# Optimization experiments

Hardware: AMD Instinct MI355X
Metric: run time of the kernel (lower is better)

The kernel has to match this reference:

```python
import jax, jax.numpy as jnp
import numpy as np

N, E = 50000, 1600000
F_IN, EDGE_DIM, HID, HEADS, NCLS = 64, 16, 128, 4, 40
C = HID // HEADS  # per-head dim = 32


def setup_inputs() -> dict:
    key = jax.random.key(0)
    ks = jax.random.split(key, 20)
    s = 0.1
    inp = {
        'x': jax.random.normal(ks[0], (N, F_IN), jnp.float32),
        'edge_index': jax.random.randint(ks[1], (2, E), 0, N, jnp.int64),
        'edge_attr': jax.random.normal(ks[2], (E, EDGE_DIM), jnp.float32),
        # layer 1 params
        'W1': jax.random.normal(ks[3], (HID, F_IN), jnp.float32) * s,
        'as1': jax.random.normal(ks[4], (HEADS, C), jnp.float32) * s,
        'ad1': jax.random.normal(ks[5], (HEADS, C), jnp.float32) * s,
        'ae1': jax.random.normal(ks[6], (HEADS, C), jnp.float32) * s,
        'We1': jax.random.normal(ks[7], (HID, EDGE_DIM), jnp.float32) * s,
        'b1': jnp.zeros((HID,), jnp.float32),
        # layer 2 params
        'W2': jax.random.normal(ks[8], (HID, HID), jnp.float32) * s,
        'as2': jax.random.normal(ks[9], (HEADS, C), jnp.float32) * s,
        'ad2': jax.random.normal(ks[10], (HEADS, C), jnp.float32) * s,
        'ae2': jax.random.normal(ks[11], (HEADS, C), jnp.float32) * s,
        'We2': jax.random.normal(ks[12], (HID, EDGE_DIM), jnp.float32) * s,
        'b2': jnp.zeros((HID,), jnp.float32),
        # final classifier
        'Wlin': jax.random.normal(ks[13], (NCLS, HID), jnp.float32) * s,
        'blin': jnp.zeros((NCLS,), jnp.float32),
    }
    return inp


def gat_conv(x, src, dst, eattr, W, a_s, a_d, a_e, We, b):
    """PyG GATConv (concat=True, add_self_loops=True, fill_value='mean'), eval mode."""
    n = x.shape[0]
    H, Cd = a_s.shape
    h = (x @ W.T).reshape(n, H, Cd)  # [N,H,C]
    # self-loop edge_attr = per-destination mean of incoming edge_attr
    cnt = jax.ops.segment_sum(jnp.ones((dst.shape[0],), eattr.dtype), dst, num_segments=n)
    mean_ea = jax.ops.segment_sum(eattr, dst, num_segments=n) / jnp.maximum(cnt, 1.0)[:, None]
    loops = jnp.arange(n, dtype=src.dtype)
    s_idx = jnp.concatenate([src, loops])
    d_idx = jnp.concatenate([dst, loops])
    ea = jnp.concatenate([eattr, mean_ea], axis=0)  # [E+N, edge_dim]
    e = (ea @ We.T).reshape(-1, H, Cd)
    # edge-wise attention logits
    alpha = (h * a_s).sum(-1)[s_idx] + (h * a_d).sum(-1)[d_idx] + (e * a_e).sum(-1)  # [E+N,H]
    alpha = jax.nn.leaky_relu(alpha, 0.2)
    # segment softmax over destination neighborhoods (every node has a self-loop)
    amax = jax.ops.segment_max(alpha, d_idx, num_segments=n)
    ex = jnp.exp(alpha - amax[d_idx])
    den = jax.ops.segment_sum(ex, d_idx, num_segments=n)
    coef = ex / (den[d_idx] + 1e-16)
    out = jax.ops.segment_sum(h[s_idx] * coef[:, :, None], d_idx, num_segments=n)
    return out.reshape(n, H * Cd) + b


def reference(x, edge_index, edge_attr, W1, as1, ad1, ae1, We1, b1,
              W2, as2, ad2, ae2, We2, b2, Wlin, blin):
    src, dst = edge_index[0], edge_index[1]
    h = jax.nn.relu(gat_conv(x, src, dst, edge_attr, W1, as1, ad1, ae1, We1, b1))
    h = jax.nn.relu(gat_conv(h, src, dst, edge_attr, W2, as2, ad2, ae2, We2, b2))
    logits = h @ Wlin.T + blin
    return jax.nn.log_softmax(logits, axis=1)
```

## Files before the change

kernel.cpp:

```cpp
#include <hip/hip_runtime.h>
#include <hip/hip_bf16.h>
#include <math.h>


#define CHUNK 2048

typedef __attribute__((ext_vector_type(8))) short short8;
typedef __attribute__((ext_vector_type(4))) float floatx4;
typedef __attribute__((ext_vector_type(2))) float floatx2;

__device__ __forceinline__ unsigned short f2bf(float f) {
  unsigned u = __float_as_uint(f);
  unsigned r = u + 0x7FFFu + ((u >> 16) & 1u);
  return (unsigned short)(r >> 16);
}
__device__ __forceinline__ float bf2f(unsigned short b) {
  return __uint_as_float(((unsigned)b) << 16);
}

__global__ __launch_bounds__(512) void hist_kernel(const int* __restrict__ dst,
                                                   int* __restrict__ bucketCnt,
                                                   int* __restrict__ chunkHist,
                                                   int E, int NB) {
  __shared__ int hist[512];
  const int tid = threadIdx.x;
  hist[tid] = 0;
  __syncthreads();
  const int e0 = blockIdx.x * CHUNK, e1 = min(e0 + CHUNK, E);
  for (int e = e0 + tid; e < e1; e += 512) atomicAdd(&hist[dst[e] >> 7], 1);
  __syncthreads();
  chunkHist[(size_t)blockIdx.x * 512 + tid] = hist[tid];
  if (tid < NB && hist[tid]) atomicAdd(&bucketCnt[tid], hist[tid]);
}

__global__ __launch_bounds__(512) void scanB_kernel(const int* __restrict__ bucketCnt,
                                                    int* __restrict__ bucketOffs,
                                                    int* __restrict__ bucketPos,
                                                    int* __restrict__ offs,
                                                    int NB, int N, int E) {
  __shared__ int sc[512];
  const int tid = threadIdx.x;
  const int v = (tid < NB) ? bucketCnt[tid] : 0;
  sc[tid] = v;
  __syncthreads();
  for (int off = 1; off < 512; off <<= 1) {
    int t = (tid >= off) ? sc[tid - off] : 0;
    __syncthreads();
    sc[tid] += t;
    __syncthreads();
  }
  const int excl = sc[tid] - v;
  if (tid < NB) { bucketOffs[tid] = excl; bucketPos[tid] = excl; }
  if (tid == 0) { bucketOffs[NB] = E; offs[N] = E; }
}

__global__ __launch_bounds__(512) void partB_kernel(const int* __restrict__ src,
                                                    const int* __restrict__ dst,
                                                    const float* __restrict__ ea,
                                                    const float* __restrict__ ae1,
                                                    const float* __restrict__ We1,
                                                    const float* __restrict__ ae2,
                                                    const float* __restrict__ We2,
                                                    const int* __restrict__ chunkHist,
                                                    int* __restrict__ bucketPos,
                                                    int4* __restrict__ binned16,
                                                    int* __restrict__ binned4,
                                                    unsigned char* __restrict__ dlArr,
                                                    int E, int NB) {
  __shared__ float wa[128];
  __shared__ int lbase[513], gbase[512], lcnt[512];
  __shared__ int waveSum[8];
  __shared__ int4 stg16[CHUNK];
  __shared__ int stg4[CHUNK];
  const int tid = threadIdx.x;
  const int wv = tid >> 6;
  const int lane = tid & 63;
  const int e0 = blockIdx.x * CHUNK;
  const int e1 = min(e0 + CHUNK, E);
  lcnt[tid] = 0;
  if (tid < 128) {
    const float* aev = (tid < 64) ? ae1 : ae2;
    const float* Wev = (tid < 64) ? We1 : We2;
    const int h = (tid >> 4) & 3;
    const int d = tid & 15;
    float s = 0.f;
#pragma unroll
    for (int c = 0; c < 32; ++c) s += aev[h * 32 + c] * Wev[(h * 32 + c) * 16 + d];
    wa[tid] = s;
  }
  const int hv = chunkHist[(size_t)blockIdx.x * 512 + tid];
  int v = hv;
#pragma unroll
  for (int off = 1; off < 64; off <<= 1) {
    int t = __shfl_up(v, off);
    if (lane >= off) v += t;
  }
  if (lane == 63) waveSum[wv] = v;
  __syncthreads();
  int woff = 0;
#pragma unroll
  for (int i = 0; i < 8; ++i) woff += (i < wv) ? waveSum[i] : 0;
  const int incl = v + woff;
  lbase[tid + 1] = incl;
  if (tid == 0) lbase[0] = 0;
  if (tid < NB && hv > 0) gbase[tid] = atomicAdd(&bucketPos[tid], hv);
  __syncthreads();
  for (int e = e0 + tid; e < e1; e += 512) {
    const int d = dst[e];
    const int b = d >> 7;
    const int lr = atomicAdd(&lcnt[b], 1);
    const float4* p = (const float4*)(ea + (size_t)e * 16);
    float4 q0 = p[0], q1 = p[1], q2 = p[2], q3 = p[3];
    float v16[16] = {q0.x, q0.y, q0.z, q0.w, q1.x, q1.y, q1.z, q1.w,
                     q2.x, q2.y, q2.z, q2.w, q3.x, q3.y, q3.z, q3.w};
    unsigned short rr[8];
#pragma unroll
    for (int h = 0; h < 8; ++h) {
      float sm = 0.f;
#pragma unroll
      for (int d2 = 0; d2 < 16; ++d2) sm += v16[d2] * wa[h * 16 + d2];
      rr[h] = f2bf(sm);
    }
    int4 pv;
    pv.x = (int)(((unsigned)(src[e] & 0xFFFF)) | ((unsigned)(d & 127) << 16) |
                 ((unsigned)b << 23));
    pv.y = (int)(((unsigned)rr[1] << 16) | rr[0]);
    pv.z = (int)(((unsigned)rr[3] << 16) | rr[2]);
    pv.w = (int)(((unsigned)rr[5] << 16) | rr[4]);
    const int sp = lbase[b] + lr;
    stg16[sp] = pv;
    stg4[sp] = (int)(((unsigned)rr[7] << 16) | rr[6]);
  }
  __syncthreads();
  const int total = e1 - e0;
  for (int t = tid; t < total; t += 512) {
    const int4 pv = stg16[t];
    const int b = (int)(((unsigned)pv.x) >> 23);
    const int g = gbase[b] + (t - lbase[b]);
    binned16[g] = pv;
    binned4[g] = stg4[t];
    dlArr[g] = (unsigned char)((pv.x >> 16) & 127);
  }
}

__global__ __launch_bounds__(256) void passC_kernel(const int4* __restrict__ binned16,
                                                    const int* __restrict__ binned4,
                                                    const unsigned char* __restrict__ dlArr,
                                                    const int* __restrict__ bucketOffs,
                                                    int* __restrict__ srcS,
                                                    uint2* __restrict__ aeS1,
                                                    uint2* __restrict__ aeS2,
                                                    int* __restrict__ offs, int N) {
  __shared__ int cnt[128], dbase[129], dpos[128];
  const int tid = threadIdx.x;
  const int b = blockIdx.x;
  const int bo = bucketOffs[b], be = bucketOffs[b + 1];
  const int m = be - bo;
  if (tid < 128) { cnt[tid] = 0; dpos[tid] = 0; }
  __syncthreads();
  for (int t = tid; t < m; t += 256) atomicAdd(&cnt[dlArr[bo + t]], 1);
  __syncthreads();
  for (int off = 1; off < 128; off <<= 1) {
    int t = (tid < 128 && tid >= (unsigned)off) ? cnt[tid - off] : 0;
    __syncthreads();
    if (tid < 128) cnt[tid] += t;
    __syncthreads();
  }
  if (tid == 0) dbase[0] = 0;
  if (tid < 128) dbase[tid + 1] = cnt[tid];
  __syncthreads();
  const int dcnt = min(128, N - (b << 7));
  if (tid < dcnt) offs[(b << 7) + tid] = bo + dbase[tid];
  for (int t = tid; t < m; t += 256) {
    const int4 v = binned16[bo + t];
    const int w4 = binned4[bo + t];
    const int dl = (v.x >> 16) & 127;
    const int p = dbase[dl] + atomicAdd(&dpos[dl], 1);
    srcS[bo + p] = v.x & 0xFFFF;
    aeS1[bo + p] = make_uint2((unsigned)v.y, (unsigned)v.z);
    aeS2[bo + p] = make_uint2((unsigned)v.w, (unsigned)w4);
  }
}

__global__ __launch_bounds__(256) void cvtall_kernel(const float* __restrict__ W1,
                                                     unsigned short* __restrict__ Wb1,
                                                     const float* __restrict__ W2,
                                                     unsigned short* __restrict__ Wb2,
                                                     const float* __restrict__ Wlin,
                                                     unsigned short* __restrict__ whi,
                                                     unsigned short* __restrict__ wlo) {
  const int n1 = 128 * 64, n2 = 128 * 128, n3 = 48 * 128;
  int i = blockIdx.x * 256 + threadIdx.x;
  if (i < n1) {
    Wb1[i] = f2bf(W1[i]);
  } else if (i < n1 + n2) {
    Wb2[i - n1] = f2bf(W2[i - n1]);
  } else if (i < n1 + n2 + n3) {
    const int j = i - n1 - n2;
    float v = (j < 40 * 128) ? Wlin[j] : 0.f;
    unsigned short h = f2bf(v);
    whi[j] = h;
    wlo[j] = f2bf(v - bf2f(h));
  }
}

#define GEMM_MFMA_SWAPPED(KTOT, PA, PB)                                            \
  {                                                                                \
    for (int kc = 0; kc < (KTOT); kc += 32) {                                      \
      const int koff = kc + (quad << 3);                                           \
      short8 aw[2], bx[4];                                                         \
      _Pragma("unroll") for (int ct = 0; ct < 2; ++ct)                             \
        aw[ct] = *(const short8*)(&Bs[(w * 32 + ct * 16 + l15) * (PB) + koff]);    \
      _Pragma("unroll") for (int nt_ = 0; nt_ < 4; ++nt_)                          \
        bx[nt_] = *(const short8*)(&As[(nt_ * 16 + l15) * (PA) + koff]);           \
      _Pragma("unroll") for (int ct = 0; ct < 2; ++ct)                             \
        _Pragma("unroll") for (int nt_ = 0; nt_ < 4; ++nt_)                        \
          acc[ct][nt_] =                                                           \
              __builtin_amdgcn_mfma_f32_16x16x32_bf16(aw[ct], bx[nt_],             \
                                                      acc[ct][nt_], 0, 0, 0);      \
    }                                                                              \
  }

#define GEMM_WRITE_H_SWAPPED()                                                     \
  {                                                                                \
    _Pragma("unroll") for (int nt_ = 0; nt_ < 4; ++nt_) {                          \
      const int node = m0 + nt_ * 16 + l15;                                        \
      if (node < n) {                                                              \
        _Pragma("unroll") for (int ct = 0; ct < 2; ++ct) {                         \
          const int ch = w * 32 + ct * 16 + (quad << 2);                           \
          ushort4 o;                                                               \
          o.x = f2bf(acc[ct][nt_][0]); o.y = f2bf(acc[ct][nt_][1]);                \
          o.z = f2bf(acc[ct][nt_][2]); o.w = f2bf(acc[ct][nt_][3]);                \
          *(ushort4*)(H + (size_t)node * 128 + ch) = o;                            \
        }                                                                          \
      }                                                                            \
    }                                                                              \
  }

#define GEMM_SCORE_SWAPPED()                                                       \
  {                                                                                \
    float asv[2][4], adv[2][4];                                                    \
    _Pragma("unroll") for (int ct = 0; ct < 2; ++ct)                               \
      _Pragma("unroll") for (int r = 0; r < 4; ++r) {                              \
        const int c = w * 32 + ct * 16 + (quad << 2) + r;                          \
        asv[ct][r] = a_s[c]; adv[ct][r] = a_d[c];                                  \
      }                                                                            \
    _Pragma("unroll") for (int nt_ = 0; nt_ < 4; ++nt_) {                          \
      float ps = 0.f, pd = 0.f;                                                    \
      _Pragma("unroll") for (int ct = 0; ct < 2; ++ct)                             \
        _Pragma("unroll") for (int r = 0; r < 4; ++r) {                            \
          ps += acc[ct][nt_][r] * asv[ct][r];                                      \
          pd += acc[ct][nt_][r] * adv[ct][r];                                      \
        }                                                                          \
      ps += __shfl_xor(ps, 16); ps += __shfl_xor(ps, 32);                          \
      pd += __shfl_xor(pd, 16); pd += __shfl_xor(pd, 32);                          \
      if (lane < 16) {                                                             \
        const int node = m0 + nt_ * 16 + lane;                                     \
        if (node < n) {                                                            \
          ssc[(size_t)node * 4 + w] = ps;                                          \
          dsc[(size_t)node * 4 + w] = pd;                                          \
        }                                                                          \
      }                                                                            \
    }                                                                              \
  }

__global__ __launch_bounds__(256) void gemm_score_f32_kernel(const float* __restrict__ X,
                                                             const unsigned short* __restrict__ Wb,
                                                             const float* __restrict__ a_s,
                                                             const float* __restrict__ a_d,
                                                             unsigned short* __restrict__ H,
                                                             float* __restrict__ ssc,
                                                             float* __restrict__ dsc,
                                                             int n) {
  __shared__ unsigned short As[64 * 72];
  __shared__ unsigned short Bs[128 * 72];
  const int tid = threadIdx.x;
  const int w = tid >> 6;
  const int lane = tid & 63;
  const int m0 = blockIdx.x * 64;
  const int quad = lane >> 4;
  const int l15 = lane & 15;

#pragma unroll
  for (int it = 0; it < 4; ++it) {
    const int idx = it * 256 + tid;
    const int row = idx >> 4;
    const int c4 = (idx & 15) * 4;
    const int grow = min(m0 + row, n - 1);
    const float4 q = *(const float4*)(X + (size_t)grow * 64 + c4);
    unsigned short* dstp = &As[row * 72 + c4];
    dstp[0] = f2bf(q.x); dstp[1] = f2bf(q.y); dstp[2] = f2bf(q.z); dstp[3] = f2bf(q.w);
  }
#pragma unroll
  for (int it = 0; it < 4; ++it) {
    const int idx = it * 256 + tid;
    const int row = idx >> 3;
    const int c8 = (idx & 7) * 8;
    short8 v = *(const short8*)(Wb + (size_t)row * 64 + c8);
    *(short8*)(&Bs[row * 72 + c8]) = v;
  }
  __syncthreads();

  floatx4 acc[2][4];
#pragma unroll
  for (int ct = 0; ct < 2; ++ct)
#pragma unroll
    for (int nt_ = 0; nt_ < 4; ++nt_) acc[ct][nt_] = (floatx4)(0.f);

  GEMM_MFMA_SWAPPED(64, 72, 72)
  GEMM_WRITE_H_SWAPPED()
  GEMM_SCORE_SWAPPED()
}

__global__ __launch_bounds__(256) void gemm_score_kernel(const unsigned short* __restrict__ X,
                                                         const unsigned short* __restrict__ Wb,
                                                         const float* __restrict__ a_s,
                                                         const float* __restrict__ a_d,
                                                         unsigned short* __restrict__ H,
                                                         float* __restrict__ ssc,
                                                         float* __restrict__ dsc,
                                                         int n) {
  __shared__ unsigned short As[64 * 136];
  __shared__ unsigned short Bs[128 * 136];
  const int tid = threadIdx.x;
  const int w = tid >> 6;
  const int lane = tid & 63;
  const int m0 = blockIdx.x * 64;
  const int quad = lane >> 4;
  const int l15 = lane & 15;

#pragma unroll
  for (int it = 0; it < 4; ++it) {
    const int idx = it * 256 + tid;
    const int row = idx >> 4;
    const int c8 = (idx & 15) * 8;
    const int grow = min(m0 + row, n - 1);
    short8 v = *(const short8*)(X + (size_t)grow * 128 + c8);
    *(short8*)(&As[row * 136 + c8]) = v;
  }
#pragma unroll
  for (int it = 0; it < 8; ++it) {
    const int idx = it * 256 + tid;
    const int row = idx >> 4;
    const int c8 = (idx & 15) * 8;
    short8 v = *(const short8*)(Wb + (size_t)row * 128 + c8);
    *(short8*)(&Bs[row * 136 + c8]) = v;
  }
  __syncthreads();

  floatx4 acc[2][4];
#pragma unroll
  for (int ct = 0; ct < 2; ++ct)
#pragma unroll
    for (int nt_ = 0; nt_ < 4; ++nt_) acc[ct][nt_] = (floatx4)(0.f);

  GEMM_MFMA_SWAPPED(128, 136, 136)
  GEMM_WRITE_H_SWAPPED()
  GEMM_SCORE_SWAPPED()
}

__device__ __forceinline__ float leaky02(float a) { return a > 0.f ? a : 0.2f * a; }
__device__ __forceinline__ float sel4(float4 v, int h) {
  return (h == 0) ? v.x : (h == 1) ? v.y : (h == 2) ? v.z : v.w;
}

__global__ __launch_bounds__(256) void agg_kernel(const unsigned short* __restrict__ hin,
                                                  const float* __restrict__ ssc,
                                                  const float* __restrict__ dsc,
                                                  const unsigned short* __restrict__ aeS,
                                                  const int* __restrict__ offs,
                                                  const int* __restrict__ srcS,
                                                  const float* __restrict__ bias,
                                                  unsigned short* __restrict__ hout, int n) {
  __shared__ int sbuf[4][64];
  __shared__ float pbuf[4][256];
  const int tid = threadIdx.x;
  const int wv = tid >> 6;
  const int lane = tid & 63;
  const int node = blockIdx.x * 4 + wv;
  if (node >= n) return;
  const int l32 = lane & 31;
  const int half = lane >> 5;
  const int ch4 = l32 * 4;
  const int headB = l32 >> 3;
  const float4 dv = *(const float4*)(dsc + (size_t)node * 4);
  float4 l4 = make_float4(0.f, 0.f, 0.f, 0.f);
  float4 sa = make_float4(0.f, 0.f, 0.f, 0.f);
  floatx2 acc01 = (floatx2)(0.f);
  floatx2 acc23 = (floatx2)(0.f);
  const int j0 = offs[node], j1 = offs[node + 1];

  for (int jc = j0; jc < j1; jc += 64) {
    const int len = min(64, j1 - jc);
    float4 p4 = make_float4(0.f, 0.f, 0.f, 0.f);
    int sv = 0;
    if (lane < len) {
      const int j = jc + lane;
      sv = srcS[j];
      const ushort4 aq = *(const ushort4*)(aeS + (size_t)j * 4);
      const float4 ae4 = make_float4(bf2f(aq.x), bf2f(aq.y), bf2f(aq.z), bf2f(aq.w));
      const float4 ss4 = *(const float4*)(ssc + (size_t)sv * 4);
      sa.x += ae4.x; sa.y += ae4.y; sa.z += ae4.z; sa.w += ae4.w;
      p4.x = __expf(leaky02(ss4.x + dv.x + ae4.x));
      p4.y = __expf(leaky02(ss4.y + dv.y + ae4.y));
      p4.z = __expf(leaky02(ss4.z + dv.z + ae4.z));
      p4.w = __expf(leaky02(ss4.w + dv.w + ae4.w));
    }
    sbuf[wv][lane] = sv;
    *(float4*)(&pbuf[wv][lane * 4]) = p4;
    l4.x += p4.x; l4.y += p4.y; l4.z += p4.z; l4.w += p4.w;
    int k = 0;
    for (; k + 8 <= len; k += 8) {
      int s[4];
      float p[4];
      uint2 d[4];
#pragma unroll
      for (int u = 0; u < 4; ++u) {
        const int kk = k + 2 * u + half;
        s[u] = sbuf[wv][kk];
        p[u] = pbuf[wv][kk * 4 + headB];
      }
#pragma unroll
      for (int u = 0; u < 4; ++u)
        d[u] = *(const uint2*)(hin + (size_t)s[u] * 128 + ch4);
#pragma unroll
      for (int u = 0; u < 4; ++u) {
        floatx2 p2; p2.x = p[u]; p2.y = p[u];
        floatx2 h01, h23;
        h01.x = __uint_as_float(d[u].x << 16);
        h01.y = __uint_as_float(d[u].x & 0xFFFF0000u);
        h23.x = __uint_as_float(d[u].y << 16);
        h23.y = __uint_as_float(d[u].y & 0xFFFF0000u);
        acc01 += p2 * h01;
        acc23 += p2 * h23;
      }
    }
    for (; k < len; k += 2) {
      int kk = k + half;
      if (kk < len) {
        int s = sbuf[wv][kk];
        float p = pbuf[wv][kk * 4 + headB];
        uint2 d = *(const uint2*)(hin + (size_t)s * 128 + ch4);
        floatx2 p2; p2.x = p; p2.y = p;
        floatx2 h01, h23;
        h01.x = __uint_as_float(d.x << 16);
        h01.y = __uint_as_float(d.x & 0xFFFF0000u);
        h23.x = __uint_as_float(d.y << 16);
        h23.y = __uint_as_float(d.y & 0xFFFF0000u);
        acc01 += p2 * h01;
        acc23 += p2 * h23;
      }
    }
  }

  float acc[4] = {acc01.x, acc01.y, acc23.x, acc23.y};
#pragma unroll
  for (int off = 32; off; off >>= 1) {
    sa.x += __shfl_xor(sa.x, off);
    sa.y += __shfl_xor(sa.y, off);
    sa.z += __shfl_xor(sa.z, off);
    sa.w += __shfl_xor(sa.w, off);
    l4.x += __shfl_xor(l4.x, off);
    l4.y += __shfl_xor(l4.y, off);
    l4.z += __shfl_xor(l4.z, off);
    l4.w += __shfl_xor(l4.w, off);
  }
#pragma unroll
  for (int i = 0; i < 4; ++i) acc[i] += __shfl_xor(acc[i], 32);

  const int deg = j1 - j0;
  const float invd = 1.f / fmaxf((float)deg, 1.f);
  const float ssn = ssc[(size_t)node * 4 + headB];
  const float aloop = leaky02(ssn + sel4(dv, headB) + sel4(sa, headB) * invd);
  const float pl = __expf(aloop);
  const float lF = sel4(l4, headB) + pl;
  const uint2 hd = *(const uint2*)(hin + (size_t)node * 128 + ch4);
  const float hv0 = __uint_as_float(hd.x << 16);
  const float hv1 = __uint_as_float(hd.x & 0xFFFF0000u);
  const float hv2 = __uint_as_float(hd.y << 16);
  const float hv3 = __uint_as_float(hd.y & 0xFFFF0000u);
  const float inv = 1.f / (lF + 1e-16f);
  const float4 bi = *(const float4*)(bias + ch4);
  const float o0 = fmaxf((acc[0] + pl * hv0) * inv + bi.x, 0.f);
  const float o1 = fmaxf((acc[1] + pl * hv1) * inv + bi.y, 0.f);
  const float o2 = fmaxf((acc[2] + pl * hv2) * inv + bi.z, 0.f);
  const float o3 = fmaxf((acc[3] + pl * hv3) * inv + bi.w, 0.f);
  if (half == 0) {
    ushort4 o;
    o.x = f2bf(o0); o.y = f2bf(o1); o.z = f2bf(o2); o.w = f2bf(o3);
    *(ushort4*)(hout + (size_t)node * 128 + ch4) = o;
  }
}

__global__ __launch_bounds__(256) void classifier_kernel(const unsigned short* __restrict__ h,
                                                         const unsigned short* __restrict__ Whi,
                                                         const unsigned short* __restrict__ Wlo,
                                                         const float* __restrict__ blin,
                                                         float* __restrict__ out, int n) {
  const int w = threadIdx.x >> 6;
  const int lane = threadIdx.x & 63;
  const int quad = lane >> 4;
  const int l15 = lane & 15;
  const int row0 = blockIdx.x * 64 + w * 16;
  if (row0 >= n) return;
  int rowm = row0 + l15;
  if (rowm >= n) rowm = n - 1;
  floatx4 acc[3];
#pragma unroll
  for (int nt = 0; nt < 3; ++nt) acc[nt] = (floatx4)(0.f);
  const size_t hbase = (size_t)rowm * 128;
#pragma unroll
  for (int kc = 0; kc < 128; kc += 32) {
    const int koff = kc + (quad << 3);
    short8 a = *(const short8*)(h + hbase + koff);
#pragma unroll
    for (int nt = 0; nt < 3; ++nt) {
      short8 bh = *(const short8*)(Whi + (size_t)(nt * 16 + l15) * 128 + koff);
      short8 bl = *(const short8*)(Wlo + (size_t)(nt * 16 + l15) * 128 + koff);
      acc[nt] = __builtin_amdgcn_mfma_f32_16x16x32_bf16(a, bh, acc[nt], 0, 0, 0);
      acc[nt] = __builtin_amdgcn_mfma_f32_16x16x32_bf16(a, bl, acc[nt], 0, 0, 0);
    }
  }
  const float bl0 = blin[l15];
  const float bl1 = blin[16 + l15];
  const float bl2 = (l15 < 8) ? blin[32 + l15] : 0.f;
#pragma unroll
  for (int r = 0; r < 4; ++r) {
    const int rrow = row0 + (quad << 2) + r;
    const float v0 = acc[0][r] + bl0;
    const float v1 = acc[1][r] + bl1;
    const float v2 = (l15 < 8) ? (acc[2][r] + bl2) : -INFINITY;
    float m = fmaxf(v0, fmaxf(v1, v2));
#pragma unroll
    for (int off = 8; off; off >>= 1) m = fmaxf(m, __shfl_xor(m, off, 16));
    const float e2 = (l15 < 8) ? __expf(v2 - m) : 0.f;
    float s = __expf(v0 - m) + __expf(v1 - m) + e2;
#pragma unroll
    for (int off = 8; off; off >>= 1) s += __shfl_xor(s, off, 16);
    const float ls = m + __logf(s);
    if (rrow < n) {
      float* po = out + (size_t)rrow * 40;
      po[l15] = v0 - ls;
      po[16 + l15] = v1 - ls;
      if (l15 < 8) po[32 + l15] = v2 - ls;
    }
  }
}

extern "C" void kernel_launch(void* const* d_in, const int* in_sizes, int n_in,
                              void* d_out, int out_size, void* d_ws, size_t ws_size,
                              hipStream_t stream) {
  const float* x    = (const float*)d_in[0];
  const int*   eidx = (const int*)d_in[1];
  const float* ea   = (const float*)d_in[2];
  const float* W1   = (const float*)d_in[3];
  const float* as1  = (const float*)d_in[4];
  const float* ad1  = (const float*)d_in[5];
  const float* ae1w = (const float*)d_in[6];
  const float* We1  = (const float*)d_in[7];
  const float* b1   = (const float*)d_in[8];
  const float* W2   = (const float*)d_in[9];
  const float* as2  = (const float*)d_in[10];
  const float* ad2  = (const float*)d_in[11];
  const float* ae2w = (const float*)d_in[12];
  const float* We2  = (const float*)d_in[13];
  const float* b2   = (const float*)d_in[14];
  const float* Wlin = (const float*)d_in[15];
  const float* blin = (const float*)d_in[16];
  float* out = (float*)d_out;

  const int N = in_sizes[0] / 64;
  const int E = in_sizes[1] / 2;
  const int* src = eidx;
  const int* dst = eidx + E;
  const int NB = (N + 127) >> 7;
  const int gp = (E + CHUNK - 1) / CHUNK;

  char* wsb = (char*)d_ws;
  size_t off = 0;
  auto alloc = [&](size_t bytes) -> void* {
    void* p = wsb + off;
    off = (off + bytes + 255) & ~(size_t)255;
    return p;
  };
  int* bucketCnt  = (int*)alloc(512 * 4);
  int* bucketOffs = (int*)alloc(513 * 4);
  int* bucketPos  = (int*)alloc(512 * 4);
  int* offs       = (int*)alloc((size_t)(N + 1) * 4);
  int* chunkHist  = (int*)alloc((size_t)gp * 512 * 4);
  uint2* aeS1     = (uint2*)alloc((size_t)E * 8);
  uint2* aeS2     = (uint2*)alloc((size_t)E * 8);
  void* regC      = alloc((size_t)E * 16);
  int4* binned16  = (int4*)regC;
  unsigned short* hA = (unsigned short*)regC;
  int* binned4    = (int*)alloc((size_t)E * 4);
  unsigned char* dlArr = (unsigned char*)alloc((size_t)E);
  int* srcS       = (int*)alloc((size_t)E * 4);
  unsigned short* Wb1 = (unsigned short*)alloc(128 * 64 * 2);
  unsigned short* Wb2 = (unsigned short*)alloc(128 * 128 * 2);
  unsigned short* Wlh = (unsigned short*)alloc(48 * 128 * 2);
  unsigned short* Wll = (unsigned short*)alloc(48 * 128 * 2);
  float* ssc      = (float*)alloc((size_t)N * 4 * 4);
  float* dsc      = (float*)alloc((size_t)N * 4 * 4);
  unsigned short* hB = (unsigned short*)alloc((size_t)N * 128 * 2);

  const int gg = (N + 63) / 64;
  const int gs = (N + 3) / 4;
  const int ncvt = 128 * 64 + 128 * 128 + 48 * 128;

  hipMemsetAsync(bucketCnt, 0, 512 * 4, stream);
  hist_kernel<<<gp, 512, 0, stream>>>(dst, bucketCnt, chunkHist, E, NB);
  scanB_kernel<<<1, 512, 0, stream>>>(bucketCnt, bucketOffs, bucketPos, offs, NB, N, E);
  partB_kernel<<<gp, 512, 0, stream>>>(src, dst, ea, ae1w, We1, ae2w, We2, chunkHist,
                                       bucketPos, binned16, binned4, dlArr, E, NB);
  passC_kernel<<<NB, 256, 0, stream>>>(binned16, binned4, dlArr, bucketOffs, srcS,
                                       aeS1, aeS2, offs, N);

  cvtall_kernel<<<(ncvt + 255) / 256, 256, 0, stream>>>(W1, Wb1, W2, Wb2, Wlin, Wlh, Wll);

  gemm_score_f32_kernel<<<gg, 256, 0, stream>>>(x, Wb1, as1, ad1, hA, ssc, dsc, N);
  agg_kernel<<<gs, 256, 0, stream>>>(hA, ssc, dsc, (const unsigned short*)aeS1, offs, srcS, b1, hB, N);

  gemm_score_kernel<<<gg, 256, 0, stream>>>(hB, Wb2, as2, ad2, hA, ssc, dsc, N);
  agg_kernel<<<gs, 256, 0, stream>>>(hA, ssc, dsc, (const unsigned short*)aeS2, offs, srcS, b2, hB, N);

  classifier_kernel<<<gg, 256, 0, stream>>>(hB, Wlh, Wll, blin, out, N);
}
```

Baseline: 458.1 us.

## Compute CSR offsets via global degree count and scan; prefetch edges in partB

Replaces the per-bucket local histogram and scan in passC (which read a separate per-edge dlArr byte array) with a global per-node degree count done with atomics, followed by a three-kernel multi-block scan that produces CSR offsets directly. passC then uses these global offsets and drops its shared-memory histogram. partB also software-pipelines its edge loop by loading the next edge's dst, src and attributes before processing the current one. The change removes the dlArr write and read, but adds a 1.6M-atomic count pass, a memset and several small kernel launches.

```diff
diff --git a/kernel.cpp b/kernel.cpp
--- a/kernel.cpp
+++ b/kernel.cpp
@@ -52,6 +52,53 @@
   const int excl = sc[tid] - v;
   if (tid < NB) { bucketOffs[tid] = excl; bucketPos[tid] = excl; }
   if (tid == 0) { bucketOffs[NB] = E; offs[N] = E; }
+}
+
+__global__ __launch_bounds__(256) void countN_kernel(const int* __restrict__ dst,
+                                                     int* __restrict__ cnt, int E) {
+  int i = blockIdx.x * 256 + threadIdx.x;
+  const int stride = gridDim.x * 256;
+  for (; i < E; i += stride) atomicAdd(&cnt[dst[i]], 1);
+}
+
+__global__ __launch_bounds__(256) void scanA_kernel(const int* __restrict__ cnt,
+                                                    int* __restrict__ offs,
+                                                    int* __restrict__ blockSum, int N) {
+  __shared__ int sc[256];
+  const int tid = threadIdx.x;
+  const int i = blockIdx.x * 256 + tid;
+  const int v = (i < N) ? cnt[i] : 0;
+  sc[tid] = v;
+  __syncthreads();
+  for (int off = 1; off < 256; off <<= 1) {
+    int t = (tid >= off) ? sc[tid - off] : 0;
+    __syncthreads();
+    sc[tid] += t;
+    __syncthreads();
+  }
+  if (i < N) offs[i] = sc[tid] - v;
+  if (tid == 255) blockSum[blockIdx.x] = sc[255];
+}
+
+__global__ __launch_bounds__(256) void scanBlk_kernel(int* __restrict__ blockSum, int NBLK) {
+  __shared__ int sc[256];
+  const int tid = threadIdx.x;
+  const int v = (tid < NBLK) ? blockSum[tid] : 0;
+  sc[tid] = v;
+  __syncthreads();
+  for (int off = 1; off < 256; off <<= 1) {
+    int t = (tid >= off) ? sc[tid - off] : 0;
+    __syncthreads();
+    sc[tid] += t;
+    __syncthreads();
+  }
+  if (tid < NBLK) blockSum[tid] = sc[tid] - v;
+}
+
+__global__ __launch_bounds__(256) void finz_kernel(int* __restrict__ offs,
+                                                   const int* __restrict__ blockSum, int N) {
+  const int i = blockIdx.x * 256 + threadIdx.x;
+  if (i < N) offs[i] += blockSum[i >> 8];
 }
 
 __global__ __launch_bounds__(512) void partB_kernel(const int* __restrict__ src,
@@ -65,7 +112,6 @@
                                                     int* __restrict__ bucketPos,
                                                     int4* __restrict__ binned16,
                                                     int* __restrict__ binned4,
-                                                    unsigned char* __restrict__ dlArr,
                                                     int E, int NB) {
   __shared__ float wa[128];
   __shared__ int lbase[513], gbase[512], lcnt[512];
@@ -100,36 +146,54 @@
   int woff = 0;
 #pragma unroll
   for (int i = 0; i < 8; ++i) woff += (i < wv) ? waveSum[i] : 0;
-  const int incl = v + woff;
-  lbase[tid + 1] = incl;
+  lbase[tid + 1] = v + woff;
   if (tid == 0) lbase[0] = 0;
   if (tid < NB && hv > 0) gbase[tid] = atomicAdd(&bucketPos[tid], hv);
   __syncthreads();
-  for (int e = e0 + tid; e < e1; e += 512) {
-    const int d = dst[e];
-    const int b = d >> 7;
-    const int lr = atomicAdd(&lcnt[b], 1);
-    const float4* p = (const float4*)(ea + (size_t)e * 16);
-    float4 q0 = p[0], q1 = p[1], q2 = p[2], q3 = p[3];
-    float v16[16] = {q0.x, q0.y, q0.z, q0.w, q1.x, q1.y, q1.z, q1.w,
-                     q2.x, q2.y, q2.z, q2.w, q3.x, q3.y, q3.z, q3.w};
-    unsigned short rr[8];
-#pragma unroll
-    for (int h = 0; h < 8; ++h) {
-      float sm = 0.f;
-#pragma unroll
-      for (int d2 = 0; d2 < 16; ++d2) sm += v16[d2] * wa[h * 16 + d2];
-      rr[h] = f2bf(sm);
+  {
+    int e = e0 + tid;
+    bool valid = (e < e1);
+    int dcur = 0, scur = 0;
+    float4 qa, qb, qc, qd;
+    if (valid) {
+      dcur = dst[e]; scur = src[e];
+      const float4* p = (const float4*)(ea + (size_t)e * 16);
+      qa = p[0]; qb = p[1]; qc = p[2]; qd = p[3];
     }
-    int4 pv;
-    pv.x = (int)(((unsigned)(src[e] & 0xFFFF)) | ((unsigned)(d & 127) << 16) |
-                 ((unsigned)b << 23));
-    pv.y = (int)(((unsigned)rr[1] << 16) | rr[0]);
-    pv.z = (int)(((unsigned)rr[3] << 16) | rr[2]);
-    pv.w = (int)(((unsigned)rr[5] << 16) | rr[4]);
-    const int sp = lbase[b] + lr;
-    stg16[sp] = pv;
-    stg4[sp] = (int)(((unsigned)rr[7] << 16) | rr[6]);
+    while (valid) {
+      const int en = e + 512;
+      const bool vnext = (en < e1);
+      int dnxt = 0, snxt = 0;
+      float4 na, nb, nc, nd;
+      if (vnext) {
+        dnxt = dst[en]; snxt = src[en];
+        const float4* p = (const float4*)(ea + (size_t)en * 16);
+        na = p[0]; nb = p[1]; nc = p[2]; nd = p[3];
+      }
+      const int b = dcur >> 7;
+      const int lr = atomicAdd(&lcnt[b], 1);
+      float v16[16] = {qa.x, qa.y, qa.z, qa.w, qb.x, qb.y, qb.z, qb.w,
+                       qc.x, qc.y, qc.z, qc.w, qd.x, qd.y, qd.z, qd.w};
+      unsigned short rr[8];
+#pragma unroll
+      for (int h = 0; h < 8; ++h) {
+        float sm = 0.f;
+#pragma unroll
+        for (int d2 = 0; d2 < 16; ++d2) sm += v16[d2] * wa[h * 16 + d2];
+        rr[h] = f2bf(sm);
+      }
+      int4 pv;
+      pv.x = (int)(((unsigned)(scur & 0xFFFF)) | ((unsigned)(dcur & 127) << 16) |
+                   ((unsigned)b << 23));
+      pv.y = (int)(((unsigned)rr[1] << 16) | rr[0]);
+      pv.z = (int)(((unsigned)rr[3] << 16) | rr[2]);
+      pv.w = (int)(((unsigned)rr[5] << 16) | rr[4]);
+      const int sp = lbase[b] + lr;
+      stg16[sp] = pv;
+      stg4[sp] = (int)(((unsigned)rr[7] << 16) | rr[6]);
+      e = en; valid = vnext; dcur = dnxt; scur = snxt;
+      qa = na; qb = nb; qc = nc; qd = nd;
+    }
   }
   __syncthreads();
   const int total = e1 - e0;
@@ -139,46 +203,35 @@
     const int g = gbase[b] + (t - lbase[b]);
     binned16[g] = pv;
     binned4[g] = stg4[t];
-    dlArr[g] = (unsigned char)((pv.x >> 16) & 127);
   }
 }
 
 __global__ __launch_bounds__(256) void passC_kernel(const int4* __restrict__ binned16,
                                                     const int* __restrict__ binned4,
-                                                    const unsigned char* __restrict__ dlArr,
                                                     const int* __restrict__ bucketOffs,
+                                                    const int* __restrict__ offs,
                                                     int* __restrict__ srcS,
                                                     uint2* __restrict__ aeS1,
-                                                    uint2* __restrict__ aeS2,
-                                                    int* __restrict__ offs, int N) {
-  __shared__ int cnt[128], dbase[129], dpos[128];
+                                                    uint2* __restrict__ aeS2, int N) {
+  __shared__ int dbaseG[128], dpos[128];
   const int tid = threadIdx.x;
   const int b = blockIdx.x;
   const int bo = bucketOffs[b], be = bucketOffs[b + 1];
   const int m = be - bo;
-  if (tid < 128) { cnt[tid] = 0; dpos[tid] = 0; }
-  __syncthreads();
-  for (int t = tid; t < m; t += 256) atomicAdd(&cnt[dlArr[bo + t]], 1);
-  __syncthreads();
-  for (int off = 1; off < 128; off <<= 1) {
-    int t = (tid < 128 && tid >= (unsigned)off) ? cnt[tid - off] : 0;
-    __syncthreads();
-    if (tid < 128) cnt[tid] += t;
-    __syncthreads();
-  }
-  if (tid == 0) dbase[0] = 0;
-  if (tid < 128) dbase[tid + 1] = cnt[tid];
-  __syncthreads();
   const int dcnt = min(128, N - (b << 7));
-  if (tid < dcnt) offs[(b << 7) + tid] = bo + dbase[tid];
+  if (tid < 128) {
+    dpos[tid] = 0;
+    dbaseG[tid] = (tid < dcnt) ? offs[(b << 7) + tid] : 0;
+  }
+  __syncthreads();
   for (int t = tid; t < m; t += 256) {
     const int4 v = binned16[bo + t];
     const int w4 = binned4[bo + t];
     const int dl = (v.x >> 16) & 127;
-    const int p = dbase[dl] + atomicAdd(&dpos[dl], 1);
-    srcS[bo + p] = v.x & 0xFFFF;
-    aeS1[bo + p] = make_uint2((unsigned)v.y, (unsigned)v.z);
-    aeS2[bo + p] = make_uint2((unsigned)v.w, (unsigned)w4);
+    const int p = dbaseG[dl] + atomicAdd(&dpos[dl], 1);
+    srcS[p] = v.x & 0xFFFF;
+    aeS1[p] = make_uint2((unsigned)v.y, (unsigned)v.z);
+    aeS2[p] = make_uint2((unsigned)v.w, (unsigned)w4);
   }
 }
 
@@ -575,6 +628,7 @@
   const int* dst = eidx + E;
   const int NB = (N + 127) >> 7;
   const int gp = (E + CHUNK - 1) / CHUNK;
+  const int NBLK = (N + 255) / 256;
 
   char* wsb = (char*)d_ws;
   size_t off = 0;
@@ -587,6 +641,8 @@
   int* bucketOffs = (int*)alloc(513 * 4);
   int* bucketPos  = (int*)alloc(512 * 4);
   int* offs       = (int*)alloc((size_t)(N + 1) * 4);
+  int* degCnt     = (int*)alloc((size_t)N * 4);
+  int* blockSum   = (int*)alloc(256 * 4);
   int* chunkHist  = (int*)alloc((size_t)gp * 512 * 4);
   uint2* aeS1     = (uint2*)alloc((size_t)E * 8);
   uint2* aeS2     = (uint2*)alloc((size_t)E * 8);
@@ -594,7 +650,6 @@
   int4* binned16  = (int4*)regC;
   unsigned short* hA = (unsigned short*)regC;
   int* binned4    = (int*)alloc((size_t)E * 4);
-  unsigned char* dlArr = (unsigned char*)alloc((size_t)E);
   int* srcS       = (int*)alloc((size_t)E * 4);
   unsigned short* Wb1 = (unsigned short*)alloc(128 * 64 * 2);
   unsigned short* Wb2 = (unsigned short*)alloc(128 * 128 * 2);
@@ -606,15 +661,21 @@
 
   const int gg = (N + 63) / 64;
   const int gs = (N + 3) / 4;
+  const int ge = (E + 255) / 256;
   const int ncvt = 128 * 64 + 128 * 128 + 48 * 128;
 
   hipMemsetAsync(bucketCnt, 0, 512 * 4, stream);
+  hipMemsetAsync(degCnt, 0, (size_t)N * 4, stream);
   hist_kernel<<<gp, 512, 0, stream>>>(dst, bucketCnt, chunkHist, E, NB);
+  countN_kernel<<<2048, 256, 0, stream>>>(dst, degCnt, E);
   scanB_kernel<<<1, 512, 0, stream>>>(bucketCnt, bucketOffs, bucketPos, offs, NB, N, E);
+  scanA_kernel<<<NBLK, 256, 0, stream>>>(degCnt, offs, blockSum, N);
+  scanBlk_kernel<<<1, 256, 0, stream>>>(blockSum, NBLK);
+  finz_kernel<<<NBLK, 256, 0, stream>>>(offs, blockSum, N);
   partB_kernel<<<gp, 512, 0, stream>>>(src, dst, ea, ae1w, We1, ae2w, We2, chunkHist,
-                                       bucketPos, binned16, binned4, dlArr, E, NB);
-  passC_kernel<<<NB, 256, 0, stream>>>(binned16, binned4, dlArr, bucketOffs, srcS,
-                                       aeS1, aeS2, offs, N);
+                                       bucketPos, binned16, binned4, E, NB);
+  passC_kernel<<<NB, 256, 0, stream>>>(binned16, binned4, bucketOffs, offs,
+                                       srcS, aeS1, aeS2, N);
 
   cvtall_kernel<<<(ncvt + 255) / 256, 256, 0, stream>>>(W1, Wb1, W2, Wb2, Wlin, Wlh, Wll);
 
```

New measurement: 521.4 us. +13.8%, slower.
